# Optimization experiments

Measured on AMD Instinct MI355X. Metric: run time of the kernel, lower is better.

Reference implementation:

```python
import jax, jax.numpy as jnp
import numpy as np

LOG_STD_MAX = 2.0
LOG_STD_MIN = -5.0
HEIGHT = 4          # tree height -> 16 leaves, 15 internal nodes
TOP_K = 4           # top-k leaves kept in soft gate
SMAX_TEMP = 1.0     # softmax temperature over selected leaf logits


def _path_matrix(height: int) -> np.ndarray:
    """[N_internal, L] matrix with +1 where a leaf's root-to-leaf path goes
    left through a node, -1 where it goes right, 0 otherwise."""
    L = 2 ** height
    P = np.zeros((L - 1, L), dtype=np.float32)
    for leaf in range(L):
        node = 0
        for lvl in range(height):
            bit = (leaf >> (height - 1 - lvl)) & 1
            P[node, leaf] = 1.0 if bit == 0 else -1.0
            node = 2 * node + 1 + bit
    return P


def setup_inputs() -> dict:
    key = jax.random.key(0)
    k0, k1, k2, k3, k4 = jax.random.split(key, 5)
    B, D, A = 262144, 128, 8
    L = 2 ** HEIGHT
    N = L - 1
    x = jax.random.normal(k0, (B, D), dtype=jnp.float32)
    Wn = jax.random.normal(k1, (D, N), dtype=jnp.float32) / np.float32(np.sqrt(D))
    bn = jax.random.normal(k2, (N,), dtype=jnp.float32) * 0.01
    Wl = jax.random.normal(k3, (L, D, 2 * A), dtype=jnp.float32) / np.float32(np.sqrt(D))
    bl = jax.random.normal(k4, (L, 2 * A), dtype=jnp.float32) * 0.01
    return {"x": x, "Wn": Wn, "bn": bn, "Wl": Wl, "bl": bl}


def reference(x, Wn, bn, Wl, bl):
    L = Wl.shape[0]
    P = jnp.asarray(_path_matrix(HEIGHT))              # [N, L] constant

    # --- differentiable-tree routing ---
    node_logits = x @ Wn + bn                          # [B, N]
    leaf_logits = node_logits @ P                      # [B, L]
    vals, idx = jax.lax.top_k(leaf_logits, TOP_K)      # [B, k]
    soft = jax.nn.softmax(vals / SMAX_TEMP, axis=-1)   # [B, k]
    onehot = jax.nn.one_hot(idx, L, dtype=x.dtype)     # [B, k, L]
    gate_soft = jnp.einsum('bk,bkl->bl', soft, onehot) # scatter soft weights
    gate_hard = onehot[:, 0]                           # argmax leaf one-hot
    # hard argmax forward, top-k softmax gradient (straight-through)
    gate = gate_hard + gate_soft - jax.lax.stop_gradient(gate_soft)

    # --- per-leaf linear controllers, gated sum ---
    leaf_out = jnp.einsum('bd,ldo->blo', x, Wl) + bl   # [B, L, 2A]
    out = jnp.einsum('bl,blo->bo', gate, leaf_out)     # [B, 2A]

    A = out.shape[-1] // 2
    mean, log_std = out[:, :A], out[:, A:]
    log_std = jnp.tanh(log_std)
    log_std = LOG_STD_MIN + 0.5 * (LOG_STD_MAX - LOG_STD_MIN) * (log_std + 1.0)
    return mean, log_std
```

## Files before the change

### kernel.cpp

```cpp
#include <hip/hip_runtime.h>
#include <math.h>

#define BLK  256
#define DD   128
#define NN   15
#define NL   16
#define OC   16
#define OSTR 20
#define GAPTHR 1e-3f

typedef __attribute__((ext_vector_type(8))) short short8v;
typedef __attribute__((ext_vector_type(4))) float f32x4;
typedef union { unsigned u[4]; short8v s; } fragu;

__device__ inline unsigned bf16_rne_u(float f) {
    unsigned u = __float_as_uint(f);
    return (u + 0x7FFFu + ((u >> 16) & 1u)) >> 16;
}
__device__ inline unsigned cvt_pk_bf16(float a, float b) {
    unsigned r;
    asm volatile("v_cvt_pk_bf16_f32 %0, %1, %2" : "=v"(r) : "v"(a), "v"(b));
    return r;
}
__device__ inline void split8(const float v[8], short8v& hi, short8v& lo) {
    fragu H, L;
    #pragma unroll
    for (int p = 0; p < 4; ++p) {
        const float a = v[2*p], b = v[2*p+1];
        const unsigned h = cvt_pk_bf16(a, b);
        H.u[p] = h;
        const float ra = a - __uint_as_float(h << 16);
        const float rb = b - __uint_as_float(h & 0xFFFF0000u);
        L.u[p] = cvt_pk_bf16(ra, rb);
    }
    hi = H.s; lo = L.s;
}

__global__ __launch_bounds__(256)
void dts_prep(const float* __restrict__ Wn, const float* __restrict__ Wl,
              unsigned short* __restrict__ wlB,
              unsigned short* __restrict__ wnHi, unsigned short* __restrict__ wnLo)
{
    const int id = blockIdx.x * 256 + threadIdx.x;
    if (id < 32768) {
        const int j = id & 7, n = (id >> 3) & 15, g = (id >> 7) & 3,
                  c = (id >> 9) & 3, leaf = id >> 11;
        const int k = c * 32 + g * 8 + j;
        wlB[id] = (unsigned short)bf16_rne_u(Wl[((size_t)leaf * DD + k) * OC + n]);
    } else if (id < 32768 + 2048) {
        const int id2 = id - 32768;
        const int j = id2 & 7, n = (id2 >> 3) & 15, g = (id2 >> 7) & 3, c = id2 >> 9;
        const int k = c * 32 + g * 8 + j;
        const float v = (n < NN) ? Wn[k * NN + n] : 0.f;
        const unsigned hb = bf16_rne_u(v);
        wnHi[id2] = (unsigned short)hb;
        wnLo[id2] = (unsigned short)bf16_rne_u(v - __uint_as_float(hb << 16));
    }
}

__global__ __launch_bounds__(BLK, 4)
void dts_fused14(const float* __restrict__ x, const float* __restrict__ Wn,
                 const float* __restrict__ bn, const float* __restrict__ bl,
                 const unsigned short* __restrict__ wlB,
                 const unsigned short* __restrict__ wnHi,
                 const unsigned short* __restrict__ wnLo,
                 float* __restrict__ out, int B)
{
    __shared__ __align__(16) float sXch[BLK * OSTR];
    __shared__ float sBn[NN];
    __shared__ __align__(16) float sBl[NL * OC];
    __shared__ unsigned char sLeaf[BLK];

    const int t    = threadIdx.x;
    const int wv   = t >> 6;
    const int lane = t & 63;
    const int lo16 = t & 15;
    const int grp  = (t >> 4) & 3;
    const int rowBase = blockIdx.x * BLK;

    if (t < NN) sBn[t] = bn[t];
    for (int i = t; i < NL * OC; i += BLK) sBl[i] = bl[i];
    __syncthreads();

    const int waveRow0 = rowBase + wv * 64;
    short8v ah[4][4];
    f32x4 accn[4];
    #pragma unroll
    for (int i = 0; i < 4; ++i) accn[i] = (f32x4){0.f, 0.f, 0.f, 0.f};

    #pragma unroll
    for (int c = 0; c < 4; ++c) {
        const short8v bh = *(const short8v*)&wnHi[(c * 64 + lane) * 8];
        const short8v bw = *(const short8v*)&wnLo[(c * 64 + lane) * 8];
        #pragma unroll
        for (int i = 0; i < 4; ++i) {
            const float* ap = x + (size_t)(waveRow0 + i * 16 + lo16) * DD + c * 32 + grp * 8;
            const float4 a0 = *(const float4*)ap;
            const float4 a1 = *(const float4*)(ap + 4);
            float av[8];
            av[0]=a0.x; av[1]=a0.y; av[2]=a0.z; av[3]=a0.w;
            av[4]=a1.x; av[5]=a1.y; av[6]=a1.z; av[7]=a1.w;
            short8v hi, lo;
            split8(av, hi, lo);
            ah[c][i] = hi;
            accn[i] = __builtin_amdgcn_mfma_f32_16x16x32_bf16(hi, bh, accn[i], 0, 0, 0);
            accn[i] = __builtin_amdgcn_mfma_f32_16x16x32_bf16(lo, bh, accn[i], 0, 0, 0);
            accn[i] = __builtin_amdgcn_mfma_f32_16x16x32_bf16(hi, bw, accn[i], 0, 0, 0);
        }
        __builtin_amdgcn_sched_barrier(0);
    }

    {
        float* patch = &sXch[wv * 64 * OSTR];
        #pragma unroll
        for (int i = 0; i < 4; ++i)
            #pragma unroll
            for (int j = 0; j < 4; ++j)
                patch[(i * 16 + grp * 4 + j) * OSTR + lo16] = accn[i][j];
    }
    asm volatile("s_waitcnt lgkmcnt(0)" ::: "memory");
    __builtin_amdgcn_sched_barrier(0);

    float nl[16];
    {
        const float4* np = (const float4*)&sXch[t * OSTR];
        const float4 n0 = np[0], n1 = np[1], n2 = np[2], n3 = np[3];
        nl[0]=n0.x; nl[1]=n0.y; nl[2]=n0.z;  nl[3]=n0.w;
        nl[4]=n1.x; nl[5]=n1.y; nl[6]=n1.z;  nl[7]=n1.w;
        nl[8]=n2.x; nl[9]=n2.y; nl[10]=n2.z; nl[11]=n2.w;
        nl[12]=n3.x; nl[13]=n3.y; nl[14]=n3.z;
    }
    #pragma unroll
    for (int n = 0; n < NN; ++n) nl[n] += sBn[n];

    float L2a[4], L3a[8], L4a[16];
    #define EXPAND(src) { \
        float p = src[0], m = -src[0]; \
        L2a[0] = p + src[1]; L2a[1] = p - src[1]; \
        L2a[2] = m + src[2]; L2a[3] = m - src[2]; \
        _Pragma("unroll") \
        for (int i = 0; i < 4; ++i) { L3a[2*i] = L2a[i] + src[3+i]; L3a[2*i+1] = L2a[i] - src[3+i]; } \
        _Pragma("unroll") \
        for (int i = 0; i < 8; ++i) { L4a[2*i] = L3a[i] + src[7+i]; L4a[2*i+1] = L3a[i] - src[7+i]; } }
    EXPAND(nl)
    int best = 0; float bv = L4a[0], sv = -1e30f;
    #pragma unroll
    for (int l = 1; l < NL; ++l) {
        if (L4a[l] > bv) { sv = bv; bv = L4a[l]; best = l; }
        else if (L4a[l] > sv) sv = L4a[l];
    }

    if (bv - sv < GAPTHR) {
        float e[NN];
        #pragma unroll
        for (int n = 0; n < NN; ++n) e[n] = 0.f;
        const float* xrow = x + (size_t)(rowBase + t) * DD;
        for (int d = 0; d < DD; ++d) {
            const float xd = xrow[d];
            const float* wr = Wn + d * NN;
            #pragma unroll
            for (int n = 0; n < NN; ++n) e[n] = fmaf(xd, wr[n], e[n]);
        }
        #pragma unroll
        for (int n = 0; n < NN; ++n) e[n] += sBn[n];
        EXPAND(e)
        best = 0; bv = L4a[0];
        #pragma unroll
        for (int l = 1; l < NL; ++l) if (L4a[l] > bv) { bv = L4a[l]; best = l; }
    }
    #undef EXPAND

    sLeaf[t] = (unsigned char)best;
    asm volatile("s_waitcnt lgkmcnt(0)" ::: "memory");
    __builtin_amdgcn_sched_barrier(0);

    unsigned lfp[4];
    #pragma unroll
    for (int rt = 0; rt < 4; ++rt)
        lfp[rt] = *(const unsigned*)&sLeaf[wv * 64 + rt * 16 + grp * 4];

    f32x4 keep[4];
    #pragma unroll
    for (int rt = 0; rt < 4; ++rt) keep[rt] = (f32x4){0.f, 0.f, 0.f, 0.f};

    #pragma unroll 1
    for (int nt = 0; nt < NL; ++nt) {
        short8v bf[4];
        #pragma unroll
        for (int c = 0; c < 4; ++c)
            bf[c] = *(const short8v*)&wlB[nt * 2048 + (c * 64 + lane) * 8];
        f32x4 acc[4];
        #pragma unroll
        for (int rt = 0; rt < 4; ++rt) acc[rt] = (f32x4){0.f, 0.f, 0.f, 0.f};
        #pragma unroll
        for (int c = 0; c < 4; ++c)
            #pragma unroll
            for (int rt = 0; rt < 4; ++rt)
                acc[rt] = __builtin_amdgcn_mfma_f32_16x16x32_bf16(ah[c][rt], bf[c], acc[rt], 0, 0, 0);
        #pragma unroll
        for (int rt = 0; rt < 4; ++rt)
            #pragma unroll
            for (int j = 0; j < 4; ++j)
                keep[rt][j] = (((lfp[rt] >> (8 * j)) & 0xFFu) == (unsigned)nt)
                            ? acc[rt][j] : keep[rt][j];
    }

    {
        float* patch = &sXch[wv * 64 * OSTR];
        #pragma unroll
        for (int rt = 0; rt < 4; ++rt)
            #pragma unroll
            for (int j = 0; j < 4; ++j) {
                const int lf = (lfp[rt] >> (8 * j)) & 0xFF;
                patch[(rt * 16 + grp * 4 + j) * OSTR + lo16] =
                    keep[rt][j] + sBl[lf * OC + lo16];
            }
    }
    asm volatile("s_waitcnt lgkmcnt(0)" ::: "memory");
    __builtin_amdgcn_sched_barrier(0);
    {
        const float* so = &sXch[t * OSTR];
        const float4 m0 = *(const float4*)(so);
        const float4 m1 = *(const float4*)(so + 4);
        const float4 s0 = *(const float4*)(so + 8);
        const float4 s1 = *(const float4*)(so + 12);

        const size_t ob = (size_t)(rowBase + t) * 8;
        *reinterpret_cast<float4*>(&out[ob])     = m0;
        *reinterpret_cast<float4*>(&out[ob + 4]) = m1;

        float4 r0, r1;
        #define SQ(v) (-1.5f + 3.5f * (1.f - 2.f / (__expf(2.f * (v)) + 1.f)))
        r0.x = SQ(s0.x); r0.y = SQ(s0.y); r0.z = SQ(s0.z); r0.w = SQ(s0.w);
        r1.x = SQ(s1.x); r1.y = SQ(s1.y); r1.z = SQ(s1.z); r1.w = SQ(s1.w);
        #undef SQ
        const size_t ob2 = (size_t)B * 8 + ob;
        *reinterpret_cast<float4*>(&out[ob2])     = r0;
        *reinterpret_cast<float4*>(&out[ob2 + 4]) = r1;
    }
}

extern "C" void kernel_launch(void* const* d_in, const int* in_sizes, int n_in,
                              void* d_out, int out_size, void* d_ws, size_t ws_size,
                              hipStream_t stream)
{
    const float* x  = (const float*)d_in[0];
    const float* Wn = (const float*)d_in[1];
    const float* bn = (const float*)d_in[2];
    const float* Wl = (const float*)d_in[3];
    const float* bl = (const float*)d_in[4];
    float* out = (float*)d_out;

    unsigned short* wlB  = (unsigned short*)d_ws;
    unsigned short* wnHi = wlB + 32768;
    unsigned short* wnLo = wnHi + 2048;

    const int B = in_sizes[0] / DD;
    const int blocks = (B + BLK - 1) / BLK;

    hipLaunchKernelGGL(dts_prep, dim3(136), dim3(256), 0, stream, Wn, Wl, wlB, wnHi, wnLo);
    hipLaunchKernelGGL(dts_fused14, dim3(blocks), dim3(BLK), 0, stream,
                       x, Wn, bn, bl, wlB, wnHi, wnLo, out, B);
}
```

Baseline: 60.80 us.

## Halve rows per wave to 32 and double occupancy target

Each wave now handles 32 rows instead of 64 (128 rows per block), which halves the A-fragment and accumulator register arrays. Launch bounds are raised to 8 blocks per SIMD pair so more waves can hide memory latency. The routing step now runs on only half the lanes, and the output stage uses a block-wide sync with two threads per row. In exchange, each row's leaf-weight fragments are reused across fewer rows, so wlB is reloaded twice as often per row, and half the lanes sit idle during routing.

Measured after the change: 80.36 us. +32.2%, slower.

```diff
diff --git a/kernel.cpp b/kernel.cpp
--- a/kernel.cpp
+++ b/kernel.cpp
@@ -2,6 +2,8 @@
 #include <math.h>
 
 #define BLK  256
+#define RPB  128
+#define RPW  32
 #define DD   128
 #define NN   15
 #define NL   16
@@ -58,42 +60,42 @@
     }
 }
 
-__global__ __launch_bounds__(BLK, 4)
-void dts_fused14(const float* __restrict__ x, const float* __restrict__ Wn,
+__global__ __launch_bounds__(BLK, 8)
+void dts_fused16(const float* __restrict__ x, const float* __restrict__ Wn,
                  const float* __restrict__ bn, const float* __restrict__ bl,
                  const unsigned short* __restrict__ wlB,
                  const unsigned short* __restrict__ wnHi,
                  const unsigned short* __restrict__ wnLo,
                  float* __restrict__ out, int B)
 {
-    __shared__ __align__(16) float sXch[BLK * OSTR];
+    __shared__ __align__(16) float sXch[RPB * OSTR];
     __shared__ float sBn[NN];
     __shared__ __align__(16) float sBl[NL * OC];
-    __shared__ unsigned char sLeaf[BLK];
+    __shared__ unsigned char sLeaf[RPB];
 
     const int t    = threadIdx.x;
     const int wv   = t >> 6;
     const int lane = t & 63;
     const int lo16 = t & 15;
     const int grp  = (t >> 4) & 3;
-    const int rowBase = blockIdx.x * BLK;
+    const int rowBase = blockIdx.x * RPB;
 
     if (t < NN) sBn[t] = bn[t];
     for (int i = t; i < NL * OC; i += BLK) sBl[i] = bl[i];
     __syncthreads();
 
-    const int waveRow0 = rowBase + wv * 64;
-    short8v ah[4][4];
-    f32x4 accn[4];
-    #pragma unroll
-    for (int i = 0; i < 4; ++i) accn[i] = (f32x4){0.f, 0.f, 0.f, 0.f};
+    const int waveRow0 = rowBase + wv * RPW;
+    short8v ah[4][2];
+    f32x4 accn[2];
+    #pragma unroll
+    for (int i = 0; i < 2; ++i) accn[i] = (f32x4){0.f, 0.f, 0.f, 0.f};
 
     #pragma unroll
     for (int c = 0; c < 4; ++c) {
         const short8v bh = *(const short8v*)&wnHi[(c * 64 + lane) * 8];
         const short8v bw = *(const short8v*)&wnLo[(c * 64 + lane) * 8];
         #pragma unroll
-        for (int i = 0; i < 4; ++i) {
+        for (int i = 0; i < 2; ++i) {
             const float* ap = x + (size_t)(waveRow0 + i * 16 + lo16) * DD + c * 32 + grp * 8;
             const float4 a0 = *(const float4*)ap;
             const float4 a1 = *(const float4*)(ap + 4);
@@ -111,9 +113,9 @@
     }
 
     {
-        float* patch = &sXch[wv * 64 * OSTR];
-        #pragma unroll
-        for (int i = 0; i < 4; ++i)
+        float* patch = &sXch[wv * RPW * OSTR];
+        #pragma unroll
+        for (int i = 0; i < 2; ++i)
             #pragma unroll
             for (int j = 0; j < 4; ++j)
                 patch[(i * 16 + grp * 4 + j) * OSTR + lo16] = accn[i][j];
@@ -121,67 +123,69 @@
     asm volatile("s_waitcnt lgkmcnt(0)" ::: "memory");
     __builtin_amdgcn_sched_barrier(0);
 
-    float nl[16];
-    {
-        const float4* np = (const float4*)&sXch[t * OSTR];
-        const float4 n0 = np[0], n1 = np[1], n2 = np[2], n3 = np[3];
-        nl[0]=n0.x; nl[1]=n0.y; nl[2]=n0.z;  nl[3]=n0.w;
-        nl[4]=n1.x; nl[5]=n1.y; nl[6]=n1.z;  nl[7]=n1.w;
-        nl[8]=n2.x; nl[9]=n2.y; nl[10]=n2.z; nl[11]=n2.w;
-        nl[12]=n3.x; nl[13]=n3.y; nl[14]=n3.z;
-    }
-    #pragma unroll
-    for (int n = 0; n < NN; ++n) nl[n] += sBn[n];
-
-    float L2a[4], L3a[8], L4a[16];
-    #define EXPAND(src) { \
-        float p = src[0], m = -src[0]; \
-        L2a[0] = p + src[1]; L2a[1] = p - src[1]; \
-        L2a[2] = m + src[2]; L2a[3] = m - src[2]; \
-        _Pragma("unroll") \
-        for (int i = 0; i < 4; ++i) { L3a[2*i] = L2a[i] + src[3+i]; L3a[2*i+1] = L2a[i] - src[3+i]; } \
-        _Pragma("unroll") \
-        for (int i = 0; i < 8; ++i) { L4a[2*i] = L3a[i] + src[7+i]; L4a[2*i+1] = L3a[i] - src[7+i]; } }
-    EXPAND(nl)
-    int best = 0; float bv = L4a[0], sv = -1e30f;
-    #pragma unroll
-    for (int l = 1; l < NL; ++l) {
-        if (L4a[l] > bv) { sv = bv; bv = L4a[l]; best = l; }
-        else if (L4a[l] > sv) sv = L4a[l];
-    }
-
-    if (bv - sv < GAPTHR) {
-        float e[NN];
-        #pragma unroll
-        for (int n = 0; n < NN; ++n) e[n] = 0.f;
-        const float* xrow = x + (size_t)(rowBase + t) * DD;
-        for (int d = 0; d < DD; ++d) {
-            const float xd = xrow[d];
-            const float* wr = Wn + d * NN;
-            #pragma unroll
-            for (int n = 0; n < NN; ++n) e[n] = fmaf(xd, wr[n], e[n]);
-        }
-        #pragma unroll
-        for (int n = 0; n < NN; ++n) e[n] += sBn[n];
-        EXPAND(e)
-        best = 0; bv = L4a[0];
-        #pragma unroll
-        for (int l = 1; l < NL; ++l) if (L4a[l] > bv) { bv = L4a[l]; best = l; }
-    }
-    #undef EXPAND
-
-    sLeaf[t] = (unsigned char)best;
+    if (lane < RPW) {
+        float nl[16];
+        {
+            const float4* np = (const float4*)&sXch[(wv * RPW + lane) * OSTR];
+            const float4 n0 = np[0], n1 = np[1], n2 = np[2], n3 = np[3];
+            nl[0]=n0.x; nl[1]=n0.y; nl[2]=n0.z;  nl[3]=n0.w;
+            nl[4]=n1.x; nl[5]=n1.y; nl[6]=n1.z;  nl[7]=n1.w;
+            nl[8]=n2.x; nl[9]=n2.y; nl[10]=n2.z; nl[11]=n2.w;
+            nl[12]=n3.x; nl[13]=n3.y; nl[14]=n3.z;
+        }
+        #pragma unroll
+        for (int n = 0; n < NN; ++n) nl[n] += sBn[n];
+
+        float L2a[4], L3a[8], L4a[16];
+        #define EXPAND(src) { \
+            float p = src[0], m = -src[0]; \
+            L2a[0] = p + src[1]; L2a[1] = p - src[1]; \
+            L2a[2] = m + src[2]; L2a[3] = m - src[2]; \
+            _Pragma("unroll") \
+            for (int i = 0; i < 4; ++i) { L3a[2*i] = L2a[i] + src[3+i]; L3a[2*i+1] = L2a[i] - src[3+i]; } \
+            _Pragma("unroll") \
+            for (int i = 0; i < 8; ++i) { L4a[2*i] = L3a[i] + src[7+i]; L4a[2*i+1] = L3a[i] - src[7+i]; } }
+        EXPAND(nl)
+        int best = 0; float bv = L4a[0], sv = -1e30f;
+        #pragma unroll
+        for (int l = 1; l < NL; ++l) {
+            if (L4a[l] > bv) { sv = bv; bv = L4a[l]; best = l; }
+            else if (L4a[l] > sv) sv = L4a[l];
+        }
+
+        if (bv - sv < GAPTHR) {
+            float e[NN];
+            #pragma unroll
+            for (int n = 0; n < NN; ++n) e[n] = 0.f;
+            const float* xrow = x + (size_t)(waveRow0 + lane) * DD;
+            for (int d = 0; d < DD; ++d) {
+                const float xd = xrow[d];
+                const float* wr = Wn + d * NN;
+                #pragma unroll
+                for (int n = 0; n < NN; ++n) e[n] = fmaf(xd, wr[n], e[n]);
+            }
+            #pragma unroll
+            for (int n = 0; n < NN; ++n) e[n] += sBn[n];
+            EXPAND(e)
+            best = 0; bv = L4a[0];
+            #pragma unroll
+            for (int l = 1; l < NL; ++l) if (L4a[l] > bv) { bv = L4a[l]; best = l; }
+        }
+        #undef EXPAND
+
+        sLeaf[wv * RPW + lane] = (unsigned char)best;
+    }
     asm volatile("s_waitcnt lgkmcnt(0)" ::: "memory");
     __builtin_amdgcn_sched_barrier(0);
 
-    unsigned lfp[4];
-    #pragma unroll
-    for (int rt = 0; rt < 4; ++rt)
-        lfp[rt] = *(const unsigned*)&sLeaf[wv * 64 + rt * 16 + grp * 4];
-
-    f32x4 keep[4];
-    #pragma unroll
-    for (int rt = 0; rt < 4; ++rt) keep[rt] = (f32x4){0.f, 0.f, 0.f, 0.f};
+    unsigned lfp[2];
+    #pragma unroll
+    for (int rt = 0; rt < 2; ++rt)
+        lfp[rt] = *(const unsigned*)&sLeaf[wv * RPW + rt * 16 + grp * 4];
+
+    f32x4 keep[2];
+    #pragma unroll
+    for (int rt = 0; rt < 2; ++rt) keep[rt] = (f32x4){0.f, 0.f, 0.f, 0.f};
 
     #pragma unroll 1
     for (int nt = 0; nt < NL; ++nt) {
@@ -189,16 +193,16 @@
         #pragma unroll
         for (int c = 0; c < 4; ++c)
             bf[c] = *(const short8v*)&wlB[nt * 2048 + (c * 64 + lane) * 8];
-        f32x4 acc[4];
-        #pragma unroll
-        for (int rt = 0; rt < 4; ++rt) acc[rt] = (f32x4){0.f, 0.f, 0.f, 0.f};
+        f32x4 acc[2];
+        #pragma unroll
+        for (int rt = 0; rt < 2; ++rt) acc[rt] = (f32x4){0.f, 0.f, 0.f, 0.f};
         #pragma unroll
         for (int c = 0; c < 4; ++c)
             #pragma unroll
-            for (int rt = 0; rt < 4; ++rt)
+            for (int rt = 0; rt < 2; ++rt)
                 acc[rt] = __builtin_amdgcn_mfma_f32_16x16x32_bf16(ah[c][rt], bf[c], acc[rt], 0, 0, 0);
         #pragma unroll
-        for (int rt = 0; rt < 4; ++rt)
+        for (int rt = 0; rt < 2; ++rt)
             #pragma unroll
             for (int j = 0; j < 4; ++j)
                 keep[rt][j] = (((lfp[rt] >> (8 * j)) & 0xFFu) == (unsigned)nt)
@@ -206,9 +210,9 @@
     }
 
     {
-        float* patch = &sXch[wv * 64 * OSTR];
-        #pragma unroll
-        for (int rt = 0; rt < 4; ++rt)
+        float* patch = &sXch[wv * RPW * OSTR];
+        #pragma unroll
+        for (int rt = 0; rt < 2; ++rt)
             #pragma unroll
             for (int j = 0; j < 4; ++j) {
                 const int lf = (lfp[rt] >> (8 * j)) & 0xFF;
@@ -216,27 +220,23 @@
                     keep[rt][j] + sBl[lf * OC + lo16];
             }
     }
-    asm volatile("s_waitcnt lgkmcnt(0)" ::: "memory");
-    __builtin_amdgcn_sched_barrier(0);
+    __syncthreads();
+
     {
-        const float* so = &sXch[t * OSTR];
-        const float4 m0 = *(const float4*)(so);
-        const float4 m1 = *(const float4*)(so + 4);
-        const float4 s0 = *(const float4*)(so + 8);
-        const float4 s1 = *(const float4*)(so + 12);
-
-        const size_t ob = (size_t)(rowBase + t) * 8;
-        *reinterpret_cast<float4*>(&out[ob])     = m0;
-        *reinterpret_cast<float4*>(&out[ob + 4]) = m1;
-
-        float4 r0, r1;
+        const int r = t >> 1;
+        const int h = (t & 1) * 4;
+        const float* so = &sXch[r * OSTR];
+        const float4 mv = *(const float4*)(so + h);
+        const float4 sv = *(const float4*)(so + 8 + h);
+
+        const size_t gro = (size_t)(rowBase + r) * 8 + h;
+        *reinterpret_cast<float4*>(&out[gro]) = mv;
+
+        float4 rv;
         #define SQ(v) (-1.5f + 3.5f * (1.f - 2.f / (__expf(2.f * (v)) + 1.f)))
-        r0.x = SQ(s0.x); r0.y = SQ(s0.y); r0.z = SQ(s0.z); r0.w = SQ(s0.w);
-        r1.x = SQ(s1.x); r1.y = SQ(s1.y); r1.z = SQ(s1.z); r1.w = SQ(s1.w);
+        rv.x = SQ(sv.x); rv.y = SQ(sv.y); rv.z = SQ(sv.z); rv.w = SQ(sv.w);
         #undef SQ
-        const size_t ob2 = (size_t)B * 8 + ob;
-        *reinterpret_cast<float4*>(&out[ob2])     = r0;
-        *reinterpret_cast<float4*>(&out[ob2 + 4]) = r1;
+        *reinterpret_cast<float4*>(&out[(size_t)B * 8 + gro]) = rv;
     }
 }
 
@@ -256,9 +256,9 @@
     unsigned short* wnLo = wnHi + 2048;
 
     const int B = in_sizes[0] / DD;
-    const int blocks = (B + BLK - 1) / BLK;
+    const int blocks = (B + RPB - 1) / RPB;
 
     hipLaunchKernelGGL(dts_prep, dim3(136), dim3(256), 0, stream, Wn, Wl, wlB, wnHi, wnLo);
-    hipLaunchKernelGGL(dts_fused14, dim3(blocks), dim3(BLK), 0, stream,
+    hipLaunchKernelGGL(dts_fused16, dim3(blocks), dim3(BLK), 0, stream,
                        x, Wn, bn, bl, wlB, wnHi, wnLo, out, B);
 }
```
